# Performance work log

Measured on AMD Instinct MI355X. Metric: run time of the kernel, lower is better.

The kernel has to match this reference:

```python
import jax, jax.numpy as jnp
import numpy as np

D_K = 32
N_HEADS = 16


def setup_inputs() -> dict:
    key = jax.random.key(0)
    ks = jax.random.split(key, 11)
    B, S, F = 32, 2048, 128
    d_k, d_v, filt = 32, 32, 3
    return {
        "q_in": jax.random.normal(ks[0], (B, S, F), jnp.float32),
        "k_in": jax.random.normal(ks[1], (B, S, F), jnp.float32),
        "v_in": jax.random.normal(ks[2], (B, S, F), jnp.float32),
        "Wq": jax.random.normal(ks[3], (F, d_k), jnp.float32) * 0.05,
        "bq": jax.random.normal(ks[4], (d_k,), jnp.float32) * 0.05,
        "Wk": jax.random.normal(ks[5], (F, d_k), jnp.float32) * 0.05,
        "bk": jax.random.normal(ks[6], (d_k,), jnp.float32) * 0.05,
        "Wv": jax.random.normal(ks[7], (F, d_v), jnp.float32) * 0.05,
        "bv": jax.random.normal(ks[8], (d_v,), jnp.float32) * 0.05,
        "Wo": jax.random.normal(ks[9], (N_HEADS * d_v, filt), jnp.float32) * 0.05,
        "bo": jax.random.normal(ks[10], (filt,), jnp.float32) * 0.05,
    }


def reference(q_in, k_in, v_in, Wq, bq, Wk, bk, Wv, bv, Wo, bo):
    # SingleAttention: Dense projections then scaled dot-product attention.
    q = q_in @ Wq + bq            # [B,S,d_k]
    k = k_in @ Wk + bk            # [B,S,d_k]
    v = v_in @ Wv + bv            # [B,S,d_v]
    scores = jnp.einsum('bqd,bkd->bqk', q, k) / jnp.sqrt(jnp.float32(D_K))
    attn = jax.nn.softmax(scores, axis=-1)
    head = jnp.einsum('bqk,bkd->bqd', attn, v)  # [B,S,d_v]
    # Original uses [SingleAttention()]*n_heads -> all heads are the SAME layer,
    # so the concat is n_heads identical copies of one head output.
    combined = jnp.tile(head, (1, 1, N_HEADS))   # [B,S,n_heads*d_v]
    return combined @ Wo + bo                    # [B,S,filter_size]
```

## Files before the change

kernel.cpp:

```cpp
#include <hip/hip_runtime.h>
#include <stdint.h>

using f16 = _Float16;
typedef _Float16 f16x8 __attribute__((ext_vector_type(8)));
typedef _Float16 f16x4 __attribute__((ext_vector_type(4)));
typedef float f32x4 __attribute__((ext_vector_type(4)));

constexpr int Bn    = 32;
constexpr int Sn    = 2048;
constexpr int Fn    = 128;
constexpr int DKn   = 32;
constexpr int NHn   = 16;
constexpr int FILTn = 3;
constexpr int Mn    = Bn * Sn;

constexpr float QSCALE = 0.1767766952966369f * 1.4426950408889634f;

constexpr int MISC_WOEFF = 0;
constexpr int MISC_BO    = 96;
constexpr int MISC_BQ    = 99;
constexpr int MISC_BK    = 131;
constexpr int MISC_BV    = 163;

#define ASYNC_COPY16(gp, lp)                                                   \
    __builtin_amdgcn_global_load_lds(                                          \
        (const __attribute__((address_space(1))) uint32_t*)(const void*)(gp),  \
        (__attribute__((address_space(3))) uint32_t*)(lp), 16, 0, 0)

#define WAIT_VM2 __builtin_amdgcn_s_waitcnt(0xF72)
#define WAIT_VM0 __builtin_amdgcn_s_waitcnt(0xF70)

__global__ __launch_bounds__(256) void prep_kernel(
    const float* __restrict__ Wq, const float* __restrict__ bq,
    const float* __restrict__ Wk, const float* __restrict__ bk,
    const float* __restrict__ Wv, const float* __restrict__ bv,
    const float* __restrict__ Wo, const float* __restrict__ bo,
    f16* __restrict__ wtg, float* __restrict__ misc)
{
    for (int idx = blockIdx.x * 256 + threadIdx.x; idx < 3 * 4096;
         idx += gridDim.x * 256) {
        const int T    = idx >> 12;
        const int r    = idx & 4095;
        const int nt   = r >> 11;
        const int ks   = (r >> 9) & 3;
        const int lane = (r >> 3) & 63;
        const int j    = r & 7;
        const int k    = ks * 32 + (lane >> 4) * 8 + j;
        const int c    = nt * 16 + (lane & 15);
        const float* W = (T == 0) ? Wq : ((T == 1) ? Wk : Wv);
        const float sc = (T == 0) ? QSCALE : 1.0f;
        wtg[idx] = (f16)(W[k * DKn + c] * sc);
    }
    if (blockIdx.x == 0) {
        const int t = threadIdx.x;
        if (t < 96) {
            const int d = t / 3, f = t - 3 * d;
            float s = 0.f;
#pragma unroll
            for (int h = 0; h < NHn; ++h) s += Wo[(h * DKn + d) * FILTn + f];
            misc[MISC_WOEFF + t] = s;
        } else if (t < 99) {
            misc[MISC_BO + (t - 96)] = bo[t - 96];
        } else if (t < 131) {
            misc[MISC_BQ + (t - 99)] = bq[t - 99] * QSCALE;
        } else if (t < 163) {
            misc[MISC_BK + (t - 131)] = bk[t - 131];
        } else if (t < 195) {
            misc[MISC_BV + (t - 163)] = bv[t - 163];
        }
    }
}

__global__ __launch_bounds__(256) void qkv_proj(
    const float* __restrict__ q_in, const float* __restrict__ k_in,
    const float* __restrict__ v_in,
    const f16* __restrict__ wtg, const float* __restrict__ misc,
    f16* __restrict__ q_ws, f16* __restrict__ k_ws, f16* __restrict__ v_ws)
{
    const int t    = threadIdx.x;
    const int w    = t >> 6;
    const int lane = t & 63;
    const int n    = lane & 15;
    const int quad = lane >> 4;
    const int T    = blockIdx.x / 512;
    const int rowA = (((blockIdx.x - T * 512) * 4 + w)) * 32;
    const int rowB = rowA + 16;
    const float* in = (T == 0) ? q_in : ((T == 1) ? k_in : v_in);

    f16x8 wf[2][4];
#pragma unroll
    for (int nt = 0; nt < 2; ++nt)
#pragma unroll
        for (int ks = 0; ks < 4; ++ks)
            wf[nt][ks] =
                *(const f16x8*)(wtg + T * 4096 + (nt * 4 + ks) * 512 + lane * 8);

    f16x8 afA[4], afB[4];
#pragma unroll
    for (int ks = 0; ks < 4; ++ks) {
        const float* pA = in + (size_t)(rowA + n) * Fn + ks * 32 + quad * 8;
        const float* pB = in + (size_t)(rowB + n) * Fn + ks * 32 + quad * 8;
        const float4 a0 = *(const float4*)pA;
        const float4 a1 = *(const float4*)(pA + 4);
        const float4 b0 = *(const float4*)pB;
        const float4 b1 = *(const float4*)(pB + 4);
        f16x8 a, b;
        a[0]=(f16)a0.x; a[1]=(f16)a0.y; a[2]=(f16)a0.z; a[3]=(f16)a0.w;
        a[4]=(f16)a1.x; a[5]=(f16)a1.y; a[6]=(f16)a1.z; a[7]=(f16)a1.w;
        b[0]=(f16)b0.x; b[1]=(f16)b0.y; b[2]=(f16)b0.z; b[3]=(f16)b0.w;
        b[4]=(f16)b1.x; b[5]=(f16)b1.y; b[6]=(f16)b1.z; b[7]=(f16)b1.w;
        afA[ks] = a;
        afB[ks] = b;
    }

    if (T < 2) {
        const float* bb = misc + (T == 0 ? MISC_BQ : MISC_BK);
        const float b0 = bb[n], b1 = bb[16 + n];
        f32x4 accA0 = {b0, b0, b0, b0}, accA1 = {b1, b1, b1, b1};
        f32x4 accB0 = {b0, b0, b0, b0}, accB1 = {b1, b1, b1, b1};
#pragma unroll
        for (int ks = 0; ks < 4; ++ks) {
            accA0 = __builtin_amdgcn_mfma_f32_16x16x32_f16(afA[ks], wf[0][ks], accA0, 0, 0, 0);
            accA1 = __builtin_amdgcn_mfma_f32_16x16x32_f16(afA[ks], wf[1][ks], accA1, 0, 0, 0);
            accB0 = __builtin_amdgcn_mfma_f32_16x16x32_f16(afB[ks], wf[0][ks], accB0, 0, 0, 0);
            accB1 = __builtin_amdgcn_mfma_f32_16x16x32_f16(afB[ks], wf[1][ks], accB1, 0, 0, 0);
        }
        f16* ows = (T == 0) ? q_ws : k_ws;
#pragma unroll
        for (int r = 0; r < 4; ++r) {
            const int ra = rowA + quad * 4 + r;
            const int rb = rowB + quad * 4 + r;
            ows[(size_t)ra * DKn + n]      = (f16)accA0[r];
            ows[(size_t)ra * DKn + 16 + n] = (f16)accA1[r];
            ows[(size_t)rb * DKn + n]      = (f16)accB0[r];
            ows[(size_t)rb * DKn + 16 + n] = (f16)accB1[r];
        }
    } else {
        f32x4 accA0 = {0.f,0.f,0.f,0.f}, accA1 = {0.f,0.f,0.f,0.f};
        f32x4 accB0 = {0.f,0.f,0.f,0.f}, accB1 = {0.f,0.f,0.f,0.f};
#pragma unroll
        for (int ks = 0; ks < 4; ++ks) {
            accA0 = __builtin_amdgcn_mfma_f32_16x16x32_f16(wf[0][ks], afA[ks], accA0, 0, 0, 0);
            accA1 = __builtin_amdgcn_mfma_f32_16x16x32_f16(wf[1][ks], afA[ks], accA1, 0, 0, 0);
            accB0 = __builtin_amdgcn_mfma_f32_16x16x32_f16(wf[0][ks], afB[ks], accB0, 0, 0, 0);
            accB1 = __builtin_amdgcn_mfma_f32_16x16x32_f16(wf[1][ks], afB[ks], accB1, 0, 0, 0);
        }
        const int b  = rowA >> 11;
        const int sA = (rowA & (Sn - 1)) + n;
        const int sB = sA + 16;
#pragma unroll
        for (int r = 0; r < 4; ++r) {
            const int d0 = quad * 4 + r;
            v_ws[((size_t)(b * DKn + d0)) * Sn + sA] =
                (f16)(accA0[r] + misc[MISC_BV + d0]);
            v_ws[((size_t)(b * DKn + 16 + d0)) * Sn + sA] =
                (f16)(accA1[r] + misc[MISC_BV + 16 + d0]);
            v_ws[((size_t)(b * DKn + d0)) * Sn + sB] =
                (f16)(accB0[r] + misc[MISC_BV + d0]);
            v_ws[((size_t)(b * DKn + 16 + d0)) * Sn + sB] =
                (f16)(accB1[r] + misc[MISC_BV + 16 + d0]);
        }
    }
}

__global__ __launch_bounds__(256, 2) void flash_mfma(
    const f16* __restrict__ q_ws, const f16* __restrict__ k_ws,
    const f16* __restrict__ v_ws,
    const float* __restrict__ misc, float* __restrict__ out)
{
    __shared__ f16 kv[3][2][2048];

    const int t    = threadIdx.x;
    const int w    = t >> 6;
    const int lane = t & 63;
    const int n    = lane & 15;
    const int quad = lane >> 4;
    const int b    = (blockIdx.x & 7) * 4 + (blockIdx.x >> 7);
    const int qt   = (blockIdx.x >> 3) & 15;

    const f16* Ksrc = k_ws + (size_t)b * Sn * DKn
                    + (size_t)(t >> 2) * DKn + (((t & 3) ^ ((t >> 3) & 3)) * 8);
    const f16* Vsrc = v_ws + (size_t)b * DKn * Sn
                    + (size_t)(t >> 3) * Sn + (((t & 7) ^ ((t >> 3) & 7)) * 8);

#define STAGE(KT, BUF)                                              \
    {                                                               \
        ASYNC_COPY16(Ksrc + (size_t)(KT) * 2048, &kv[BUF][0][w * 512]); \
        ASYNC_COPY16(Vsrc + (size_t)(KT) * 64,   &kv[BUF][1][w * 512]); \
    }

    const int qrow0 = b * Sn + qt * 128 + w * 32;
    const f16x8 qa0 = *(const f16x8*)(q_ws + (size_t)(qrow0 + n) * DKn + quad * 8);
    const f16x8 qa1 = *(const f16x8*)(q_ws + (size_t)(qrow0 + 16 + n) * DKn + quad * 8);

    int koff[4];
#pragma unroll
    for (int g = 0; g < 4; ++g)
        koff[g] = (g * 64 + n * 4 + (quad ^ ((n >> 1) & 3))) * 8;

    int voff2[2][4];
#pragma unroll
    for (int h = 0; h < 2; ++h)
#pragma unroll
        for (int s = 0; s < 4; ++s) {
            const int d  = h * 16 + n;
            const int jc = s * 2 + (quad >> 1);
            voff2[h][s] = (d * 8 + (jc ^ (d & 7))) * 8 + (quad & 1) * 4;
        }

    f32x4 o00 = {0.f, 0.f, 0.f, 0.f};
    f32x4 o01 = {0.f, 0.f, 0.f, 0.f};
    f32x4 o10 = {0.f, 0.f, 0.f, 0.f};
    f32x4 o11 = {0.f, 0.f, 0.f, 0.f};
    float l0 = 0.f, l1 = 0.f;
    const f32x4 zero = {0.f, 0.f, 0.f, 0.f};

    STAGE(0, 0)
    STAGE(1, 1)

#pragma unroll 1
    for (int kt = 0; kt < Sn / 64; ++kt) {
        const int cur = kt % 3;
        WAIT_VM2;
        __builtin_amdgcn_s_barrier();
        STAGE((kt + 2) & 31, (kt + 2) % 3)

        const f16* Kt = &kv[cur][0][0];
        const f16* Vt = &kv[cur][1][0];

        const f16x8 kb0 = *(const f16x8*)(Kt + koff[0]);
        const f16x8 kb1 = *(const f16x8*)(Kt + koff[1]);
        const f16x8 kb2 = *(const f16x8*)(Kt + koff[2]);
        const f16x8 kb3 = *(const f16x8*)(Kt + koff[3]);
        f16x4 vb[2][4];
#pragma unroll
        for (int h = 0; h < 2; ++h)
#pragma unroll
            for (int s = 0; s < 4; ++s)
                vb[h][s] = *(const f16x4*)(Vt + voff2[h][s]);

        f16x4 pa0[4], pa1[4];
#define QK_GROUP(g, kbg)                                                       \
        {                                                                      \
            const f32x4 sa =                                                   \
                __builtin_amdgcn_mfma_f32_16x16x32_f16(kbg, qa0, zero, 0, 0, 0);\
            const f32x4 sb =                                                   \
                __builtin_amdgcn_mfma_f32_16x16x32_f16(kbg, qa1, zero, 0, 0, 0);\
            const float a0 = __builtin_amdgcn_exp2f(sa[0]);                    \
            const float a1 = __builtin_amdgcn_exp2f(sa[1]);                    \
            const float a2 = __builtin_amdgcn_exp2f(sa[2]);                    \
            const float a3 = __builtin_amdgcn_exp2f(sa[3]);                    \
            l0 += (a0 + a1) + (a2 + a3);                                       \
            f16x4 ppa;                                                         \
            ppa[0] = (f16)a0; ppa[1] = (f16)a1;                                \
            ppa[2] = (f16)a2; ppa[3] = (f16)a3;                                \
            pa0[g] = ppa;                                                      \
            const float b0 = __builtin_amdgcn_exp2f(sb[0]);                    \
            const float b1 = __builtin_amdgcn_exp2f(sb[1]);                    \
            const float b2 = __builtin_amdgcn_exp2f(sb[2]);                    \
            const float b3 = __builtin_amdgcn_exp2f(sb[3]);                    \
            l1 += (b0 + b1) + (b2 + b3);                                       \
            f16x4 ppb;                                                         \
            ppb[0] = (f16)b0; ppb[1] = (f16)b1;                                \
            ppb[2] = (f16)b2; ppb[3] = (f16)b3;                                \
            pa1[g] = ppb;                                                      \
        }
        QK_GROUP(0, kb0)
        QK_GROUP(1, kb1)
        QK_GROUP(2, kb2)
        QK_GROUP(3, kb3)
#undef QK_GROUP

#pragma unroll
        for (int s = 0; s < 4; ++s) {
            o00 = __builtin_amdgcn_mfma_f32_16x16x16f16(pa0[s], vb[0][s], o00, 0, 0, 0);
            o01 = __builtin_amdgcn_mfma_f32_16x16x16f16(pa0[s], vb[1][s], o01, 0, 0, 0);
            o10 = __builtin_amdgcn_mfma_f32_16x16x16f16(pa1[s], vb[0][s], o10, 0, 0, 0);
            o11 = __builtin_amdgcn_mfma_f32_16x16x16f16(pa1[s], vb[1][s], o11, 0, 0, 0);
        }
    }
#undef STAGE
    WAIT_VM0;

    l0 += __shfl_xor(l0, 16);
    l0 += __shfl_xor(l0, 32);
    l1 += __shfl_xor(l1, 16);
    l1 += __shfl_xor(l1, 32);

    float w0f[FILTn], w1f[FILTn];
#pragma unroll
    for (int f = 0; f < FILTn; ++f) {
        w0f[f] = misc[MISC_WOEFF + n * FILTn + f];
        w1f[f] = misc[MISC_WOEFF + (16 + n) * FILTn + f];
    }
#pragma unroll
    for (int qg = 0; qg < 2; ++qg) {
        const float lf = (qg == 0) ? l0 : l1;
        const f32x4 oA = (qg == 0) ? o00 : o10;
        const f32x4 oB = (qg == 0) ? o01 : o11;
#pragma unroll
        for (int r = 0; r < 4; ++r) {
            const float inv = 1.f / __shfl(lf, quad * 4 + r);
            const float a0 = oA[r] * inv;
            const float a1 = oB[r] * inv;
#pragma unroll
            for (int f = 0; f < FILTn; ++f) {
                float v = a0 * w0f[f] + a1 * w1f[f];
                v += __shfl_xor(v, 1, 16);
                v += __shfl_xor(v, 2, 16);
                v += __shfl_xor(v, 4, 16);
                v += __shfl_xor(v, 8, 16);
                if (n == f) {
                    const int row = qrow0 + qg * 16 + quad * 4 + r;
                    out[(size_t)row * FILTn + f] = v + misc[MISC_BO + f];
                }
            }
        }
    }
}

extern "C" void kernel_launch(void* const* d_in, const int* in_sizes, int n_in,
                              void* d_out, int out_size, void* d_ws,
                              size_t ws_size, hipStream_t stream)
{
    const float* q_in = (const float*)d_in[0];
    const float* k_in = (const float*)d_in[1];
    const float* v_in = (const float*)d_in[2];
    const float* Wq   = (const float*)d_in[3];
    const float* bq   = (const float*)d_in[4];
    const float* Wk   = (const float*)d_in[5];
    const float* bk   = (const float*)d_in[6];
    const float* Wv   = (const float*)d_in[7];
    const float* bv   = (const float*)d_in[8];
    const float* Wo   = (const float*)d_in[9];
    const float* bo   = (const float*)d_in[10];
    float* out = (float*)d_out;

    f16*   ws   = (f16*)d_ws;
    f16*   q_ws = ws;
    f16*   k_ws = ws + (size_t)Mn * DKn;
    f16*   v_ws = ws + 2 * (size_t)Mn * DKn;
    f16*   wtg  = ws + 3 * (size_t)Mn * DKn;
    float* misc = (float*)(wtg + 3 * 4096);

    prep_kernel<<<16, 256, 0, stream>>>(Wq, bq, Wk, bk, Wv, bv, Wo, bo, wtg, misc);

    qkv_proj<<<3 * 512, 256, 0, stream>>>(
        q_in, k_in, v_in, wtg, misc, q_ws, k_ws, v_ws);

    flash_mfma<<<Bn * (Sn / 128), 256, 0, stream>>>(
        q_ws, k_ws, v_ws, misc, out);
}
```

Baseline: 175.5 us.

## Fold Wv and summed Wo into a 3-wide value projection before attention

Because the output projection is linear and applied after softmax-weighted averaging, Wv and the head-summed Wo are precomputed into a single 128x3 matrix, so V becomes 3 channels instead of 32. The flash kernel then stages only a 3-row V slice once per block, halves the PV MFMAs, and drops the final shuffle-reduction epilogue. qkv_proj writes far less V data. The cost is extra f16 rounding on the folded product and mostly-empty MFMA columns (only 3 of 16 used).

```diff
diff --git a/kernel.cpp b/kernel.cpp
--- a/kernel.cpp
+++ b/kernel.cpp
@@ -16,18 +16,17 @@
 
 constexpr float QSCALE = 0.1767766952966369f * 1.4426950408889634f;
 
-constexpr int MISC_WOEFF = 0;
-constexpr int MISC_BO    = 96;
-constexpr int MISC_BQ    = 99;
-constexpr int MISC_BK    = 131;
-constexpr int MISC_BV    = 163;
+constexpr int MISC_BO  = 96;
+constexpr int MISC_BQ  = 99;
+constexpr int MISC_BK  = 131;
+constexpr int MISC_BV3 = 163;
 
 #define ASYNC_COPY16(gp, lp)                                                   \
     __builtin_amdgcn_global_load_lds(                                          \
         (const __attribute__((address_space(1))) uint32_t*)(const void*)(gp),  \
         (__attribute__((address_space(3))) uint32_t*)(lp), 16, 0, 0)
 
-#define WAIT_VM2 __builtin_amdgcn_s_waitcnt(0xF72)
+#define WAIT_VM1 __builtin_amdgcn_s_waitcnt(0xF71)
 #define WAIT_VM0 __builtin_amdgcn_s_waitcnt(0xF70)
 
 __global__ __launch_bounds__(256) void prep_kernel(
@@ -37,8 +36,9 @@
     const float* __restrict__ Wo, const float* __restrict__ bo,
     f16* __restrict__ wtg, float* __restrict__ misc)
 {
-    for (int idx = blockIdx.x * 256 + threadIdx.x; idx < 3 * 4096;
-         idx += gridDim.x * 256) {
+    const int t = threadIdx.x;
+
+    for (int idx = blockIdx.x * 256 + t; idx < 2 * 4096; idx += gridDim.x * 256) {
         const int T    = idx >> 12;
         const int r    = idx & 4095;
         const int nt   = r >> 11;
@@ -47,27 +47,51 @@
         const int j    = r & 7;
         const int k    = ks * 32 + (lane >> 4) * 8 + j;
         const int c    = nt * 16 + (lane & 15);
-        const float* W = (T == 0) ? Wq : ((T == 1) ? Wk : Wv);
+        const float* W = (T == 0) ? Wq : Wk;
         const float sc = (T == 0) ? QSCALE : 1.0f;
         wtg[idx] = (f16)(W[k * DKn + c] * sc);
     }
-    if (blockIdx.x == 0) {
-        const int t = threadIdx.x;
-        if (t < 96) {
-            const int d = t / 3, f = t - 3 * d;
-            float s = 0.f;
-#pragma unroll
-            for (int h = 0; h < NHn; ++h) s += Wo[(h * DKn + d) * FILTn + f];
-            misc[MISC_WOEFF + t] = s;
-        } else if (t < 99) {
-            misc[MISC_BO + (t - 96)] = bo[t - 96];
-        } else if (t < 131) {
-            misc[MISC_BQ + (t - 99)] = bq[t - 99] * QSCALE;
-        } else if (t < 163) {
-            misc[MISC_BK + (t - 131)] = bk[t - 131];
-        } else if (t < 195) {
-            misc[MISC_BV + (t - 163)] = bv[t - 163];
-        }
+
+    if (blockIdx.x != 0) return;
+
+    __shared__ float woe[DKn * FILTn];
+    __shared__ float wv3[Fn * FILTn];
+
+    if (t < DKn * FILTn) {
+        const int d = t / FILTn, f = t - FILTn * d;
+        float s = 0.f;
+#pragma unroll
+        for (int h = 0; h < NHn; ++h) s += Wo[(h * DKn + d) * FILTn + f];
+        woe[t] = s;
+    }
+    __syncthreads();
+    for (int i = t; i < Fn * FILTn; i += 256) {
+        const int k = i / FILTn, f = i - FILTn * k;
+        float s = 0.f;
+#pragma unroll
+        for (int d = 0; d < DKn; ++d) s += Wv[k * DKn + d] * woe[d * FILTn + f];
+        wv3[i] = s;
+    }
+    __syncthreads();
+    for (int idx = t; idx < 2048; idx += 256) {
+        const int ks   = idx >> 9;
+        const int lane = (idx >> 3) & 63;
+        const int j    = idx & 7;
+        const int n    = lane & 15;
+        const int quad = lane >> 4;
+        const int k    = ks * 32 + quad * 8 + j;
+        wtg[8192 + idx] = (n < FILTn) ? (f16)wv3[k * FILTn + n] : (f16)0.f;
+    }
+    if (t < FILTn) {
+        float s = 0.f;
+#pragma unroll
+        for (int d = 0; d < DKn; ++d) s += bv[d] * woe[d * FILTn + t];
+        misc[MISC_BV3 + t] = s;
+        misc[MISC_BO + t]  = bo[t];
+    } else if (t >= 99 && t < 131) {
+        misc[MISC_BQ + (t - 99)] = bq[t - 99] * QSCALE;
+    } else if (t >= 131 && t < 163) {
+        misc[MISC_BK + (t - 131)] = bk[t - 131];
     }
 }
 
@@ -87,14 +111,6 @@
     const int rowB = rowA + 16;
     const float* in = (T == 0) ? q_in : ((T == 1) ? k_in : v_in);
 
-    f16x8 wf[2][4];
-#pragma unroll
-    for (int nt = 0; nt < 2; ++nt)
-#pragma unroll
-        for (int ks = 0; ks < 4; ++ks)
-            wf[nt][ks] =
-                *(const f16x8*)(wtg + T * 4096 + (nt * 4 + ks) * 512 + lane * 8);
-
     f16x8 afA[4], afB[4];
 #pragma unroll
     for (int ks = 0; ks < 4; ++ks) {
@@ -114,6 +130,14 @@
     }
 
     if (T < 2) {
+        f16x8 wf[2][4];
+#pragma unroll
+        for (int nt = 0; nt < 2; ++nt)
+#pragma unroll
+            for (int ks = 0; ks < 4; ++ks)
+                wf[nt][ks] =
+                    *(const f16x8*)(wtg + T * 4096 + (nt * 4 + ks) * 512 + lane * 8);
+
         const float* bb = misc + (T == 0 ? MISC_BQ : MISC_BK);
         const float b0 = bb[n], b1 = bb[16 + n];
         f32x4 accA0 = {b0, b0, b0, b0}, accA1 = {b1, b1, b1, b1};
@@ -136,29 +160,26 @@
             ows[(size_t)rb * DKn + 16 + n] = (f16)accB1[r];
         }
     } else {
-        f32x4 accA0 = {0.f,0.f,0.f,0.f}, accA1 = {0.f,0.f,0.f,0.f};
-        f32x4 accB0 = {0.f,0.f,0.f,0.f}, accB1 = {0.f,0.f,0.f,0.f};
+        f16x8 wv[4];
+#pragma unroll
+        for (int ks = 0; ks < 4; ++ks)
+            wv[ks] = *(const f16x8*)(wtg + 8192 + ks * 512 + lane * 8);
+        f32x4 accA = {0.f,0.f,0.f,0.f}, accB = {0.f,0.f,0.f,0.f};
 #pragma unroll
         for (int ks = 0; ks < 4; ++ks) {
-            accA0 = __builtin_amdgcn_mfma_f32_16x16x32_f16(wf[0][ks], afA[ks], accA0, 0, 0, 0);
-            accA1 = __builtin_amdgcn_mfma_f32_16x16x32_f16(wf[1][ks], afA[ks], accA1, 0, 0, 0);
-            accB0 = __builtin_amdgcn_mfma_f32_16x16x32_f16(wf[0][ks], afB[ks], accB0, 0, 0, 0);
-            accB1 = __builtin_amdgcn_mfma_f32_16x16x32_f16(wf[1][ks], afB[ks], accB1, 0, 0, 0);
-        }
-        const int b  = rowA >> 11;
-        const int sA = (rowA & (Sn - 1)) + n;
-        const int sB = sA + 16;
-#pragma unroll
-        for (int r = 0; r < 4; ++r) {
-            const int d0 = quad * 4 + r;
-            v_ws[((size_t)(b * DKn + d0)) * Sn + sA] =
-                (f16)(accA0[r] + misc[MISC_BV + d0]);
-            v_ws[((size_t)(b * DKn + 16 + d0)) * Sn + sA] =
-                (f16)(accA1[r] + misc[MISC_BV + 16 + d0]);
-            v_ws[((size_t)(b * DKn + d0)) * Sn + sB] =
-                (f16)(accB0[r] + misc[MISC_BV + d0]);
-            v_ws[((size_t)(b * DKn + 16 + d0)) * Sn + sB] =
-                (f16)(accB1[r] + misc[MISC_BV + 16 + d0]);
+            accA = __builtin_amdgcn_mfma_f32_16x16x32_f16(wv[ks], afA[ks], accA, 0, 0, 0);
+            accB = __builtin_amdgcn_mfma_f32_16x16x32_f16(wv[ks], afB[ks], accB, 0, 0, 0);
+        }
+        if (quad == 0) {
+            const int b  = rowA >> 11;
+            const int sA = (rowA & (Sn - 1)) + n;
+            const int sB = sA + 16;
+#pragma unroll
+            for (int r = 0; r < FILTn; ++r) {
+                const float bv3 = misc[MISC_BV3 + r];
+                v_ws[((size_t)(b * FILTn + r)) * Sn + sA] = (f16)(accA[r] + bv3);
+                v_ws[((size_t)(b * FILTn + r)) * Sn + sB] = (f16)(accB[r] + bv3);
+            }
         }
     }
 }
@@ -168,7 +189,8 @@
     const f16* __restrict__ v_ws,
     const float* __restrict__ misc, float* __restrict__ out)
 {
-    __shared__ f16 kv[3][2][2048];
+    __shared__ f16 kbuf[3][2048];
+    __shared__ f16 v2[3 * 2048];
 
     const int t    = threadIdx.x;
     const int w    = t >> 6;
@@ -180,14 +202,10 @@
 
     const f16* Ksrc = k_ws + (size_t)b * Sn * DKn
                     + (size_t)(t >> 2) * DKn + (((t & 3) ^ ((t >> 3) & 3)) * 8);
-    const f16* Vsrc = v_ws + (size_t)b * DKn * Sn
-                    + (size_t)(t >> 3) * Sn + (((t & 7) ^ ((t >> 3) & 7)) * 8);
-
-#define STAGE(KT, BUF)                                              \
-    {                                                               \
-        ASYNC_COPY16(Ksrc + (size_t)(KT) * 2048, &kv[BUF][0][w * 512]); \
-        ASYNC_COPY16(Vsrc + (size_t)(KT) * 64,   &kv[BUF][1][w * 512]); \
-    }
+    const f16* V3src = v_ws + (size_t)b * FILTn * Sn + t * 8;
+
+#define STAGE(KT, BUF) \
+    ASYNC_COPY16(Ksrc + (size_t)(KT) * 2048, &kbuf[BUF][w * 512]);
 
     const int qrow0 = b * Sn + qt * 128 + w * 32;
     const f16x8 qa0 = *(const f16x8*)(q_ws + (size_t)(qrow0 + n) * DKn + quad * 8);
@@ -198,46 +216,39 @@
     for (int g = 0; g < 4; ++g)
         koff[g] = (g * 64 + n * 4 + (quad ^ ((n >> 1) & 3))) * 8;
 
-    int voff2[2][4];
-#pragma unroll
-    for (int h = 0; h < 2; ++h)
-#pragma unroll
-        for (int s = 0; s < 4; ++s) {
-            const int d  = h * 16 + n;
-            const int jc = s * 2 + (quad >> 1);
-            voff2[h][s] = (d * 8 + (jc ^ (d & 7))) * 8 + (quad & 1) * 4;
-        }
-
-    f32x4 o00 = {0.f, 0.f, 0.f, 0.f};
-    f32x4 o01 = {0.f, 0.f, 0.f, 0.f};
-    f32x4 o10 = {0.f, 0.f, 0.f, 0.f};
-    f32x4 o11 = {0.f, 0.f, 0.f, 0.f};
+    f32x4 o0 = {0.f, 0.f, 0.f, 0.f};
+    f32x4 o1 = {0.f, 0.f, 0.f, 0.f};
     float l0 = 0.f, l1 = 0.f;
     const f32x4 zero = {0.f, 0.f, 0.f, 0.f};
 
+    ASYNC_COPY16(V3src,        &v2[0    + w * 512]);
+    ASYNC_COPY16(V3src + 2048, &v2[2048 + w * 512]);
+    ASYNC_COPY16(V3src + 4096, &v2[4096 + w * 512]);
     STAGE(0, 0)
     STAGE(1, 1)
 
 #pragma unroll 1
     for (int kt = 0; kt < Sn / 64; ++kt) {
         const int cur = kt % 3;
-        WAIT_VM2;
+        WAIT_VM1;
         __builtin_amdgcn_s_barrier();
         STAGE((kt + 2) & 31, (kt + 2) % 3)
 
-        const f16* Kt = &kv[cur][0][0];
-        const f16* Vt = &kv[cur][1][0];
+        const f16* Kt = &kbuf[cur][0];
 
         const f16x8 kb0 = *(const f16x8*)(Kt + koff[0]);
         const f16x8 kb1 = *(const f16x8*)(Kt + koff[1]);
         const f16x8 kb2 = *(const f16x8*)(Kt + koff[2]);
         const f16x8 kb3 = *(const f16x8*)(Kt + koff[3]);
-        f16x4 vb[2][4];
-#pragma unroll
-        for (int h = 0; h < 2; ++h)
-#pragma unroll
-            for (int s = 0; s < 4; ++s)
-                vb[h][s] = *(const f16x4*)(Vt + voff2[h][s]);
+
+        f16x4 vb[4];
+#pragma unroll
+        for (int s = 0; s < 4; ++s) {
+            f16x4 v = {(f16)0.f, (f16)0.f, (f16)0.f, (f16)0.f};
+            if (n < FILTn)
+                v = *(const f16x4*)(v2 + n * 2048 + kt * 64 + s * 16 + quad * 4);
+            vb[s] = v;
+        }
 
         f16x4 pa0[4], pa1[4];
 #define QK_GROUP(g, kbg)                                                       \
@@ -273,10 +284,8 @@
 
 #pragma unroll
         for (int s = 0; s < 4; ++s) {
-            o00 = __builtin_amdgcn_mfma_f32_16x16x16f16(pa0[s], vb[0][s], o00, 0, 0, 0);
-            o01 = __builtin_amdgcn_mfma_f32_16x16x16f16(pa0[s], vb[1][s], o01, 0, 0, 0);
-            o10 = __builtin_amdgcn_mfma_f32_16x16x16f16(pa1[s], vb[0][s], o10, 0, 0, 0);
-            o11 = __builtin_amdgcn_mfma_f32_16x16x16f16(pa1[s], vb[1][s], o11, 0, 0, 0);
+            o0 = __builtin_amdgcn_mfma_f32_16x16x16f16(pa0[s], vb[s], o0, 0, 0, 0);
+            o1 = __builtin_amdgcn_mfma_f32_16x16x16f16(pa1[s], vb[s], o1, 0, 0, 0);
         }
     }
 #undef STAGE
@@ -287,33 +296,17 @@
     l1 += __shfl_xor(l1, 16);
     l1 += __shfl_xor(l1, 32);
 
-    float w0f[FILTn], w1f[FILTn];
-#pragma unroll
-    for (int f = 0; f < FILTn; ++f) {
-        w0f[f] = misc[MISC_WOEFF + n * FILTn + f];
-        w1f[f] = misc[MISC_WOEFF + (16 + n) * FILTn + f];
-    }
+    const float bon = misc[MISC_BO + (n < FILTn ? n : 0)];
 #pragma unroll
     for (int qg = 0; qg < 2; ++qg) {
         const float lf = (qg == 0) ? l0 : l1;
-        const f32x4 oA = (qg == 0) ? o00 : o10;
-        const f32x4 oB = (qg == 0) ? o01 : o11;
+        const f32x4 oo = (qg == 0) ? o0 : o1;
 #pragma unroll
         for (int r = 0; r < 4; ++r) {
             const float inv = 1.f / __shfl(lf, quad * 4 + r);
-            const float a0 = oA[r] * inv;
-            const float a1 = oB[r] * inv;
-#pragma unroll
-            for (int f = 0; f < FILTn; ++f) {
-                float v = a0 * w0f[f] + a1 * w1f[f];
-                v += __shfl_xor(v, 1, 16);
-                v += __shfl_xor(v, 2, 16);
-                v += __shfl_xor(v, 4, 16);
-                v += __shfl_xor(v, 8, 16);
-                if (n == f) {
-                    const int row = qrow0 + qg * 16 + quad * 4 + r;
-                    out[(size_t)row * FILTn + f] = v + misc[MISC_BO + f];
-                }
+            if (n < FILTn) {
+                const int row = qrow0 + qg * 16 + quad * 4 + r;
+                out[(size_t)row * FILTn + n] = oo[r] * inv + bon;
             }
         }
     }
@@ -343,7 +336,7 @@
     f16*   wtg  = ws + 3 * (size_t)Mn * DKn;
     float* misc = (float*)(wtg + 3 * 4096);
 
-    prep_kernel<<<16, 256, 0, stream>>>(Wq, bq, Wk, bk, Wv, bv, Wo, bo, wtg, misc);
+    prep_kernel<<<8, 256, 0, stream>>>(Wq, bq, Wk, bk, Wv, bv, Wo, bo, wtg, misc);
 
     qkv_proj<<<3 * 512, 256, 0, stream>>>(
         q_in, k_in, v_in, wtg, misc, q_ws, k_ws, v_ws);
```

After: 177.9 us. Within noise of the previous version (+1.4%).
